# Performance work log

Measured on AMD Instinct MI355X. Metric: run time of the kernel, lower is better.

Reference implementation:

```python
import jax, jax.numpy as jnp
import numpy as np

PI = float(np.pi)
SIGMA = 1.0          # density_smearing_width
NUM_GRAPHS = 16
K_TOTAL = 16384
N_NODES = 4096


def setup_inputs() -> dict:
    key = jax.random.key(0)
    k1, k2, k3, k4, k5, k6 = jax.random.split(key, 6)
    k_vectors = jax.random.normal(k1, (K_TOTAL, 3), jnp.float32) * 2.0
    k_norm2 = jnp.sum(k_vectors * k_vectors, axis=-1)            # [K]
    k_vector_batch = jnp.sort(jax.random.randint(k2, (K_TOTAL,), 0, NUM_GRAPHS, dtype=jnp.int32))
    k0_mask = jnp.zeros((K_TOTAL,), jnp.float32)                 # no k=0 vectors
    source_feats = jax.random.normal(k3, (N_NODES, 1), jnp.float32)   # monopole charges (max_l=0)
    node_positions = jax.random.normal(k4, (N_NODES, 3), jnp.float32) * 3.0
    batch = jnp.sort(jax.random.randint(k5, (N_NODES,), 0, NUM_GRAPHS, dtype=jnp.int32))
    volume = jax.random.uniform(k6, (NUM_GRAPHS,), jnp.float32, minval=100.0, maxval=300.0)
    pbc = jnp.ones((NUM_GRAPHS, 3), dtype=bool)
    return {"k_vectors": k_vectors, "k_norm2": k_norm2, "k_vector_batch": k_vector_batch,
            "k0_mask": k0_mask, "source_feats": source_feats, "node_positions": node_positions,
            "batch": batch, "volume": volume, "pbc": pbc}


def reference(k_vectors, k_norm2, k_vector_batch, k0_mask, source_feats,
              node_positions, batch, volume, pbc):
    # pbc is all-True -> static PBC (reciprocal-space) branch.
    B = volume.shape[0]
    # [K, N] phase matrix, masked to block-diagonal (same-graph) structure
    inner = k_vectors @ node_positions.T
    mask_f = (k_vector_batch[:, None] == batch[None, :]).astype(inner.dtype)
    cosines = jnp.cos(inner) * mask_f
    sines = jnp.sin(inner) * mask_f
    # GTO (Gaussian, max_l=0) density basis Fourier transform
    fs = jnp.exp(-0.5 * (SIGMA ** 2) * k_norm2)                  # [K]
    q = source_feats[:, 0]                                       # [N] monopole coeffs
    vol_per_k = volume[k_vector_batch]                           # [K]
    pref = fs * (2.0 * PI) ** 3 / vol_per_k                      # [K]
    # assemble_fourier_series_batch: real/imag structure factors
    density = jnp.stack([cosines @ q, sines @ q], axis=-1) * pref[:, None]   # [K, 2]
    # Coulomb kernel 4*pi/k^2, zeroed at k=0
    k0_bool = k0_mask > 0.0
    k_factor = jnp.where(k0_bool, 0.0, 1.0 / jnp.where(k0_bool, 1.0, k_norm2))
    potential = 4.0 * PI * density * k_factor[:, None]           # [K, 2]
    # energy_product_batch: segment-reduce per-k energies to graphs
    per_k = 2.0 * jnp.sum(density * potential, axis=-1)          # [K]
    energy_k = jax.ops.segment_sum(per_k, k_vector_batch, num_segments=B)
    energy = 0.5 * volume * energy_k / (2.0 * PI) ** 6           # [B]
    # subtract Gaussian self-interaction (include_self_interaction=False)
    self_fields = q / (SIGMA * jnp.sqrt(2.0 * PI))
    node_energies = q * self_fields
    self_energy = jax.ops.segment_sum(node_energies, batch, num_segments=B)
    return energy - 0.5 * self_energy
```

## Files before the change

kernel.cpp:

```cpp
#include <hip/hip_runtime.h>
#include <math.h>

#define NUM_GRAPHS 16
#define PI_F 3.14159265358979323846f
#define INV_SQRT_2PI 0.3989422804014327f

__global__ void gto_init_kernel(const float* __restrict__ q,
                                const int* __restrict__ batch, int n_nodes,
                                float* __restrict__ out) {
    __shared__ float acc[NUM_GRAPHS];
    int t = threadIdx.x;
    if (t < NUM_GRAPHS) acc[t] = 0.f;
    __syncthreads();

    int chunk = (n_nodes + blockDim.x - 1) / (int)blockDim.x;
    int i0 = t * chunk;
    int i1 = min(n_nodes, i0 + chunk);
    int cur = -1;
    float sum = 0.f;
    for (int i = i0; i < i1; ++i) {
        int b = batch[i];
        float qi = q[i];
        if (b != cur) {
            if (cur >= 0) atomicAdd(&acc[cur], sum);
            cur = b;
            sum = 0.f;
        }
        sum = fmaf(qi, qi, sum);
    }
    if (cur >= 0) atomicAdd(&acc[cur], sum);
    __syncthreads();
    if (t < NUM_GRAPHS) out[t] = -0.5f * acc[t] * INV_SQRT_2PI;
}

#define WAVES_PER_BLOCK 4
#define K_PER_WAVE 8
#define K_PER_BLOCK (WAVES_PER_BLOCK * K_PER_WAVE)

__global__ void __launch_bounds__(256)
gto_energy_kernel(const float* __restrict__ kvec,
                  const float* __restrict__ knorm2,
                  const int*   __restrict__ kbatch,
                  const float* __restrict__ k0mask,
                  const float* __restrict__ q,
                  const float* __restrict__ pos,
                  const float* __restrict__ volume,
                  const int*   __restrict__ batch,
                  float* __restrict__ out, int K, int N) {
    __shared__ float gacc[NUM_GRAPHS];
    __shared__ int sstart[NUM_GRAPHS + 1];
    int t = threadIdx.x;
    if (t < NUM_GRAPHS) gacc[t] = 0.f;
    if (t <= NUM_GRAPHS) {
        int lo = 0, hi = N;
        while (lo < hi) {
            int mid = (lo + hi) >> 1;
            if (batch[mid] < t) lo = mid + 1; else hi = mid;
        }
        sstart[t] = lo;
    }
    __syncthreads();

    int wave = t >> 6;
    int lane = t & 63;
    int kbase = (blockIdx.x * WAVES_PER_BLOCK + wave) * K_PER_WAVE;

    for (int kk = 0; kk < K_PER_WAVE; ++kk) {
        int k = kbase + kk;
        if (k >= K) break;
        int g = kbatch[k];
        float kx = kvec[3 * k + 0];
        float ky = kvec[3 * k + 1];
        float kz = kvec[3 * k + 2];
        int s = sstart[g];
        int e = sstart[g + 1];

        float C = 0.f, S = 0.f;
        for (int j = s + lane; j < e; j += 64) {
            float px = pos[3 * j + 0];
            float py = pos[3 * j + 1];
            float pz = pos[3 * j + 2];
            float inner = fmaf(kx, px, fmaf(ky, py, kz * pz));
            float sv, cv;
            __sincosf(inner, &sv, &cv);
            float qj = q[j];
            C = fmaf(cv, qj, C);
            S = fmaf(sv, qj, S);
        }
        #pragma unroll
        for (int off = 32; off > 0; off >>= 1) {
            C += __shfl_xor(C, off, 64);
            S += __shfl_xor(S, off, 64);
        }
        if (lane == 0) {
            float kn2 = knorm2[k];
            float fs2 = __expf(-kn2);
            float kfac = (k0mask[k] > 0.f) ? 0.f : 1.f / kn2;
            float e_k = 4.f * PI_F * kfac * fs2 * (C * C + S * S) / volume[g];
            atomicAdd(&gacc[g], e_k);
        }
    }
    __syncthreads();
    if (t < NUM_GRAPHS && gacc[t] != 0.f) {
        atomicAdd(&out[t], gacc[t]);
    }
}

extern "C" void kernel_launch(void* const* d_in, const int* in_sizes, int n_in,
                              void* d_out, int out_size, void* d_ws, size_t ws_size,
                              hipStream_t stream) {
    const float* k_vectors  = (const float*)d_in[0];
    const float* k_norm2    = (const float*)d_in[1];
    const int*   k_batch    = (const int*)  d_in[2];
    const float* k0_mask    = (const float*)d_in[3];
    const float* src_feats  = (const float*)d_in[4];
    const float* positions  = (const float*)d_in[5];
    const int*   batch      = (const int*)  d_in[6];
    const float* volume     = (const float*)d_in[7];

    int K = in_sizes[1];
    int N = in_sizes[4];
    float* out = (float*)d_out;

    gto_init_kernel<<<1, 256, 0, stream>>>(src_feats, batch, N, out);

    int blocks = (K + K_PER_BLOCK - 1) / K_PER_BLOCK;
    gto_energy_kernel<<<blocks, 256, 0, stream>>>(
        k_vectors, k_norm2, k_batch, k0_mask, src_feats, positions,
        volume, batch, out, K, N);
}
```

Measured before the change: 91.38 us.

## Fuse self-energy init into energy kernel via extra graph blocks

Removes the separate single-block self-energy init kernel. The main kernel gets NUM_GRAPHS extra blocks that each reduce q^2 for one graph and atomically add the result, and the output is zeroed with a memset first. The per-k parameters for all eight k-vectors are also loaded into registers up front, before the shared-memory setup, instead of inside the loop. This trades a kernel launch for a memset and adds global atomics, while higher register use may cut occupancy.

```diff
diff --git a/kernel.cpp b/kernel.cpp
--- a/kernel.cpp
+++ b/kernel.cpp
@@ -5,73 +5,81 @@
 #define PI_F 3.14159265358979323846f
 #define INV_SQRT_2PI 0.3989422804014327f
 
-__global__ void gto_init_kernel(const float* __restrict__ q,
-                                const int* __restrict__ batch, int n_nodes,
-                                float* __restrict__ out) {
-    __shared__ float acc[NUM_GRAPHS];
-    int t = threadIdx.x;
-    if (t < NUM_GRAPHS) acc[t] = 0.f;
-    __syncthreads();
-
-    int chunk = (n_nodes + blockDim.x - 1) / (int)blockDim.x;
-    int i0 = t * chunk;
-    int i1 = min(n_nodes, i0 + chunk);
-    int cur = -1;
-    float sum = 0.f;
-    for (int i = i0; i < i1; ++i) {
-        int b = batch[i];
-        float qi = q[i];
-        if (b != cur) {
-            if (cur >= 0) atomicAdd(&acc[cur], sum);
-            cur = b;
-            sum = 0.f;
-        }
-        sum = fmaf(qi, qi, sum);
-    }
-    if (cur >= 0) atomicAdd(&acc[cur], sum);
-    __syncthreads();
-    if (t < NUM_GRAPHS) out[t] = -0.5f * acc[t] * INV_SQRT_2PI;
-}
-
 #define WAVES_PER_BLOCK 4
 #define K_PER_WAVE 8
 #define K_PER_BLOCK (WAVES_PER_BLOCK * K_PER_WAVE)
 
 __global__ void __launch_bounds__(256)
-gto_energy_kernel(const float* __restrict__ kvec,
-                  const float* __restrict__ knorm2,
-                  const int*   __restrict__ kbatch,
-                  const float* __restrict__ k0mask,
-                  const float* __restrict__ q,
-                  const float* __restrict__ pos,
-                  const float* __restrict__ volume,
-                  const int*   __restrict__ batch,
-                  float* __restrict__ out, int K, int N) {
+gto_fused_kernel(const float* __restrict__ kvec,
+                 const float* __restrict__ knorm2,
+                 const int*   __restrict__ kbatch,
+                 const float* __restrict__ k0mask,
+                 const float* __restrict__ q,
+                 const float* __restrict__ pos,
+                 const float* __restrict__ volume,
+                 const int*   __restrict__ batch,
+                 float* __restrict__ out, int K, int N) {
     __shared__ float gacc[NUM_GRAPHS];
-    __shared__ int sstart[NUM_GRAPHS + 1];
-    int t = threadIdx.x;
+    __shared__ int   sstart[NUM_GRAPHS + 1];
+    __shared__ float wsum[WAVES_PER_BLOCK];
+
+    int bid  = blockIdx.x;
+    int t    = threadIdx.x;
+    int wave = t >> 6;
+    int lane = t & 63;
+
+    if (bid < NUM_GRAPHS) {
+        int g = bid;
+        int lo = 0, hi = N;
+        while (lo < hi) { int mid = (lo + hi) >> 1; if (batch[mid] < g)     lo = mid + 1; else hi = mid; }
+        int s = lo;
+        lo = 0; hi = N;
+        while (lo < hi) { int mid = (lo + hi) >> 1; if (batch[mid] < g + 1) lo = mid + 1; else hi = mid; }
+        int e = lo;
+
+        float sum = 0.f;
+        for (int i = s + t; i < e; i += 256) { float qi = q[i]; sum = fmaf(qi, qi, sum); }
+        #pragma unroll
+        for (int off = 32; off > 0; off >>= 1) sum += __shfl_xor(sum, off, 64);
+        if (lane == 0) wsum[wave] = sum;
+        __syncthreads();
+        if (t == 0) {
+            float s4 = wsum[0] + wsum[1] + wsum[2] + wsum[3];
+            atomicAdd(&out[g], -0.5f * s4 * INV_SQRT_2PI);
+        }
+        return;
+    }
+
     if (t < NUM_GRAPHS) gacc[t] = 0.f;
+
+    int kbase = ((bid - NUM_GRAPHS) * WAVES_PER_BLOCK + wave) * K_PER_WAVE;
+
+    float kx[K_PER_WAVE], ky[K_PER_WAVE], kz[K_PER_WAVE];
+    float kn2[K_PER_WAVE], kmk[K_PER_WAVE];
+    int   kg[K_PER_WAVE];
+    #pragma unroll
+    for (int kk = 0; kk < K_PER_WAVE; ++kk) {
+        int k = kbase + kk; if (k > K - 1) k = K - 1;
+        kx[kk]  = kvec[3 * k + 0];
+        ky[kk]  = kvec[3 * k + 1];
+        kz[kk]  = kvec[3 * k + 2];
+        kn2[kk] = knorm2[k];
+        kmk[kk] = k0mask[k];
+        kg[kk]  = kbatch[k];
+    }
+
     if (t <= NUM_GRAPHS) {
         int lo = 0, hi = N;
-        while (lo < hi) {
-            int mid = (lo + hi) >> 1;
-            if (batch[mid] < t) lo = mid + 1; else hi = mid;
-        }
+        while (lo < hi) { int mid = (lo + hi) >> 1; if (batch[mid] < t) lo = mid + 1; else hi = mid; }
         sstart[t] = lo;
     }
     __syncthreads();
 
-    int wave = t >> 6;
-    int lane = t & 63;
-    int kbase = (blockIdx.x * WAVES_PER_BLOCK + wave) * K_PER_WAVE;
-
+    #pragma unroll
     for (int kk = 0; kk < K_PER_WAVE; ++kk) {
         int k = kbase + kk;
         if (k >= K) break;
-        int g = kbatch[k];
-        float kx = kvec[3 * k + 0];
-        float ky = kvec[3 * k + 1];
-        float kz = kvec[3 * k + 2];
+        int g = kg[kk];
         int s = sstart[g];
         int e = sstart[g + 1];
 
@@ -80,7 +88,7 @@
             float px = pos[3 * j + 0];
             float py = pos[3 * j + 1];
             float pz = pos[3 * j + 2];
-            float inner = fmaf(kx, px, fmaf(ky, py, kz * pz));
+            float inner = fmaf(kx[kk], px, fmaf(ky[kk], py, kz[kk] * pz));
             float sv, cv;
             __sincosf(inner, &sv, &cv);
             float qj = q[j];
@@ -93,10 +101,9 @@
             S += __shfl_xor(S, off, 64);
         }
         if (lane == 0) {
-            float kn2 = knorm2[k];
-            float fs2 = __expf(-kn2);
-            float kfac = (k0mask[k] > 0.f) ? 0.f : 1.f / kn2;
-            float e_k = 4.f * PI_F * kfac * fs2 * (C * C + S * S) / volume[g];
+            float fs2  = __expf(-kn2[kk]);
+            float kfac = (kmk[kk] > 0.f) ? 0.f : 1.f / kn2[kk];
+            float e_k  = 4.f * PI_F * kfac * fs2 * (C * C + S * S) / volume[g];
             atomicAdd(&gacc[g], e_k);
         }
     }
@@ -122,10 +129,10 @@
     int N = in_sizes[4];
     float* out = (float*)d_out;
 
-    gto_init_kernel<<<1, 256, 0, stream>>>(src_feats, batch, N, out);
+    hipMemsetAsync(out, 0, out_size, stream);
 
-    int blocks = (K + K_PER_BLOCK - 1) / K_PER_BLOCK;
-    gto_energy_kernel<<<blocks, 256, 0, stream>>>(
+    int kblocks = (K + K_PER_BLOCK - 1) / K_PER_BLOCK;
+    gto_fused_kernel<<<kblocks + NUM_GRAPHS, 256, 0, stream>>>(
         k_vectors, k_norm2, k_batch, k0_mask, src_feats, positions,
         volume, batch, out, K, N);
 }
```

Result: faster. 85.39 us (-6.6%).
